# Kernel tuning notes

Measured on AMD Instinct MI355X. Metric: run time of the kernel, lower is better.

## Reference

```python
import jax, jax.numpy as jnp
import numpy as np
from jax.ops import segment_sum, segment_max

N_M = 100000   # muon nodes
N_J = 100000   # jet nodes
E   = 1600000  # edges per relation (~avg degree 16)
D   = 64       # input feature dim
H   = 64       # hidden_channels
C   = 2        # num_classes

def setup_inputs():
    key = jax.random.key(0)
    ks = jax.random.split(key, 16)
    g = lambda k, shape, fan: jax.random.normal(k, shape, jnp.float32) / np.sqrt(fan).astype(np.float32)
    return {
        "x_muons": jax.random.normal(ks[0], (N_M, D), jnp.float32),
        "x_jets":  jax.random.normal(ks[1], (N_J, D), jnp.float32),
        "ei_mm": jax.random.randint(ks[2], (2, E), 0, N_M, jnp.int32),
        "ei_mj": jnp.stack([jax.random.randint(ks[3], (E,), 0, N_M, jnp.int32),
                            jax.random.randint(ks[4], (E,), 0, N_J, jnp.int32)]),
        "ei_jj": jax.random.randint(ks[5], (2, E), 0, N_J, jnp.int32),
        "gat_w_src": g(ks[6], (D, H), D),
        "gat_w_dst": g(ks[7], (D, H), D),
        "gat_att_src": g(ks[8], (H,), H),
        "gat_att_dst": g(ks[9], (H,), H),
        "gat_bias": jnp.zeros((H,), jnp.float32),
        "sage_w_l": g(ks[10], (D, H), D),
        "sage_w_r": g(ks[11], (D, H), D),
        "sage_bias": jnp.zeros((H,), jnp.float32),
        "gcn_w": g(ks[12], (D, H), D),
        "gcn_bias": jnp.zeros((H,), jnp.float32),
        "lin_w": g(ks[13], (H, C), H),
        "lin_b": jnp.zeros((C,), jnp.float32),
    }

def _add_self_loops(ei, n):
    loop = jnp.arange(n, dtype=ei.dtype)
    return jnp.concatenate([ei[0], loop]), jnp.concatenate([ei[1], loop])

def _gat(x, ei, w_src, w_dst, att_src, att_dst, bias):
    # PyG GATConv, heads=1, add_self_loops=True, negative_slope=0.2
    n = x.shape[0]
    src, dst = _add_self_loops(ei, n)
    hs = x @ w_src                      # [n, H] source-side messages
    hd = x @ w_dst                      # dst-side (attention only)
    a = jax.nn.leaky_relu((hs @ att_src)[src] + (hd @ att_dst)[dst], 0.2)
    m = segment_max(a, dst, num_segments=n)      # per-dst softmax (stable)
    ea = jnp.exp(a - m[dst])
    z = segment_sum(ea, dst, num_segments=n)
    alpha = ea / z[dst]                 # self loop guarantees z > 0
    return segment_sum(alpha[:, None] * hs[src], dst, num_segments=n) + bias

def _sage(x_src, x_dst, ei, w_l, w_r, bias):
    # PyG SAGEConv: mean aggregation, root weight, no self loops
    n = x_dst.shape[0]
    src, dst = ei[0], ei[1]
    agg = segment_sum(x_src[src], dst, num_segments=n)
    cnt = segment_sum(jnp.ones_like(dst, jnp.float32), dst, num_segments=n)
    mean = agg / jnp.maximum(cnt, 1.0)[:, None]
    return mean @ w_l + x_dst @ w_r + bias

def _gcn(x, ei, w, bias):
    # PyG GCNConv: symmetric gcn_norm on A + I
    n = x.shape[0]
    src, dst = _add_self_loops(ei, n)
    xw = x @ w
    deg = segment_sum(jnp.ones_like(dst, jnp.float32), dst, num_segments=n)
    dis = deg ** -0.5                   # deg >= 1 due to self loops
    norm = dis[src] * dis[dst]
    return segment_sum(norm[:, None] * xw[src], dst, num_segments=n) + bias

def reference(x_muons, x_jets, ei_mm, ei_mj, ei_jj,
              gat_w_src, gat_w_dst, gat_att_src, gat_att_dst, gat_bias,
              sage_w_l, sage_w_r, sage_bias, gcn_w, gcn_bias, lin_w, lin_b):
    # Original forward returns inside the layer loop -> exactly one HeteroConv layer runs.
    muons = _gat(x_muons, ei_mm, gat_w_src, gat_w_dst, gat_att_src, gat_att_dst, gat_bias)
    jets = (_sage(x_muons, x_jets, ei_mj, sage_w_l, sage_w_r, sage_bias)
            + _gcn(x_jets, ei_jj, gcn_w, gcn_bias))   # HeteroConv aggr='sum' on dst type 'jets'
    muons = jax.nn.relu(muons)
    jets = jax.nn.relu(jets)
    out = jnp.concatenate([muons, jets], axis=0)       # [N_M + N_J, H]
    return jax.nn.sigmoid(out @ lin_w + lin_b)
```

## Files before the change

### kernel.cpp

```cpp
#include <hip/hip_runtime.h>
#include <math.h>

#define N_M 100000
#define N_J 100000
#define NE  1600000
#define NTOT (3*N_M)
#define ETOT (3*NE)
#define NB_SCAN 293
#define DD  64
#define HH  64

#define NBIN 586
#define BIN_SHIFT 9
#define G1 640
#define EPB ((ETOT + G1 - 1) / G1)

__device__ __forceinline__ float lrelu(float a){ return a > 0.f ? a : 0.2f*a; }
__device__ __forceinline__ float wmax(float v){
    #pragma unroll
    for (int o = 32; o; o >>= 1) v = fmaxf(v, __shfl_xor(v, o));
    return v;
}
__device__ __forceinline__ float wsum(float v){
    #pragma unroll
    for (int o = 32; o; o >>= 1) v += __shfl_xor(v, o);
    return v;
}
__device__ __forceinline__ float sigm(float x){ return 1.f/(1.f + expf(-x)); }


__global__ void k_vdst(const float* __restrict__ w_dst, const float* __restrict__ att_dst,
                       float* __restrict__ v_dst){
    int d = threadIdx.x;
    float s = 0.f;
    for (int h = 0; h < HH; ++h) s += w_dst[d*HH + h] * att_dst[h];
    v_dst[d] = s;
}

__global__ __launch_bounds__(256) void k_muon_prep(
    const float* __restrict__ x, const float* __restrict__ w_src,
    const float* __restrict__ att_src, const float* __restrict__ v_dst,
    float* __restrict__ hs, float* __restrict__ as_, float* __restrict__ ad_)
{
    __shared__ float lw[DD*HH];
    __shared__ float latt[HH];
    __shared__ float lvd[DD];
    int tid = threadIdx.x;
    for (int i = tid; i < DD*HH; i += 256) lw[i] = w_src[i];
    if (tid < HH) latt[tid] = att_src[tid];
    if (tid < DD) lvd[tid] = v_dst[tid];
    __syncthreads();
    int row = blockIdx.x*64 + (tid >> 2);
    int q = tid & 3;
    if (row >= N_M) return;
    const float4* x4 = (const float4*)(x + (size_t)row*DD);
    float acc[16];
    #pragma unroll
    for (int f = 0; f < 16; ++f) acc[f] = 0.f;
    float adp = 0.f;
    for (int kk = 0; kk < 16; ++kk){
        float4 xv = x4[kk];
        adp += xv.x*lvd[4*kk] + xv.y*lvd[4*kk+1] + xv.z*lvd[4*kk+2] + xv.w*lvd[4*kk+3];
        float xs[4] = {xv.x, xv.y, xv.z, xv.w};
        #pragma unroll
        for (int j = 0; j < 4; ++j){
            const float* wp = lw + (4*kk + j)*HH + (q << 4);
            float xk = xs[j];
            #pragma unroll
            for (int f = 0; f < 16; ++f) acc[f] = fmaf(xk, wp[f], acc[f]);
        }
    }
    float asp = 0.f;
    #pragma unroll
    for (int f = 0; f < 16; ++f) asp += acc[f] * latt[(q<<4) + f];
    asp += __shfl_xor(asp, 1);
    asp += __shfl_xor(asp, 2);
    float* hp = hs + (size_t)row*HH + (q << 4);
    #pragma unroll
    for (int j = 0; j < 4; ++j)
        ((float4*)hp)[j] = make_float4(acc[4*j], acc[4*j+1], acc[4*j+2], acc[4*j+3]);
    if (q == 0){ as_[row] = asp; ad_[row] = adp; }
}

__global__ __launch_bounds__(256) void k_gcn_xw(
    const float* __restrict__ x, const float* __restrict__ w, float* __restrict__ xw)
{
    __shared__ float lw[DD*HH];
    int tid = threadIdx.x;
    for (int i = tid; i < DD*HH; i += 256) lw[i] = w[i];
    __syncthreads();
    int row = blockIdx.x*64 + (tid >> 2);
    int q = tid & 3;
    if (row >= N_J) return;
    const float4* x4 = (const float4*)(x + (size_t)row*DD);
    float acc[16];
    #pragma unroll
    for (int f = 0; f < 16; ++f) acc[f] = 0.f;
    for (int kk = 0; kk < 16; ++kk){
        float4 xv = x4[kk];
        float xs[4] = {xv.x, xv.y, xv.z, xv.w};
        #pragma unroll
        for (int j = 0; j < 4; ++j){
            const float* wp = lw + (4*kk + j)*HH + (q << 4);
            float xk = xs[j];
            #pragma unroll
            for (int f = 0; f < 16; ++f) acc[f] = fmaf(xk, wp[f], acc[f]);
        }
    }
    float* hp = xw + (size_t)row*HH + (q << 4);
    #pragma unroll
    for (int j = 0; j < 4; ++j)
        ((float4*)hp)[j] = make_float4(acc[4*j], acc[4*j+1], acc[4*j+2], acc[4*j+3]);
}


__device__ __forceinline__ void edge_rd(int t, const int* ei_mm, const int* ei_mj,
                                        const int* ei_jj, const int** ei, int* r, int* e){
    if (t < NE){ *r = 0; *e = t; *ei = ei_mm; }
    else if (t < 2*NE){ *r = 1; *e = t - NE; *ei = ei_mj; }
    else { *r = 2; *e = t - 2*NE; *ei = ei_jj; }
}

__global__ __launch_bounds__(256) void k_bin0(
    const int* __restrict__ ei_mm, const int* __restrict__ ei_mj,
    const int* __restrict__ ei_jj, int* __restrict__ g_bincnt)
{
    __shared__ int bh[NBIN];
    int tid = threadIdx.x;
    for (int i = tid; i < NBIN; i += 256) bh[i] = 0;
    __syncthreads();
    int t0 = blockIdx.x * EPB;
    int t1 = min(t0 + EPB, ETOT);
    for (int t = t0 + tid; t < t1; t += 256){
        const int* ei; int r, e;
        edge_rd(t, ei_mm, ei_mj, ei_jj, &ei, &r, &e);
        int bucket = r*N_M + ei[NE + e];
        atomicAdd(&bh[bucket >> BIN_SHIFT], 1);
    }
    __syncthreads();
    for (int i = tid; i < NBIN; i += 256)
        if (bh[i]) atomicAdd(&g_bincnt[i], bh[i]);
}

__global__ void k_binscan(const int* __restrict__ g_bincnt, int* __restrict__ g_binoff,
                          int* __restrict__ g_bincur, int* __restrict__ offs)
{
    int l = threadIdx.x;
    int base = l * 10;
    int v[10]; int s = 0;
    #pragma unroll
    for (int k = 0; k < 10; ++k){
        int idx = base + k;
        v[k] = (idx < NBIN) ? g_bincnt[idx] : 0;
        s += v[k];
    }
    int inc = s;
    #pragma unroll
    for (int o = 1; o < 64; o <<= 1){
        int u = __shfl_up(inc, o);
        if (l >= o) inc += u;
    }
    int ex = inc - s;
    #pragma unroll
    for (int k = 0; k < 10; ++k){
        int idx = base + k;
        if (idx < NBIN){ g_binoff[idx] = ex; g_bincur[idx] = ex; ex += v[k]; }
    }
    if (l == 63) g_binoff[NBIN] = ex;
    if (l == 0)  offs[NTOT] = ETOT;
}

__global__ __launch_bounds__(256) void k_bin1(
    const int* __restrict__ ei_mm, const int* __restrict__ ei_mj,
    const int* __restrict__ ei_jj, int* __restrict__ g_bincur,
    unsigned* __restrict__ binned)
{
    __shared__ int bh[NBIN];
    __shared__ int cb[NBIN];
    int tid = threadIdx.x;
    for (int i = tid; i < NBIN; i += 256) bh[i] = 0;
    __syncthreads();
    int t0 = blockIdx.x * EPB;
    int t1 = min(t0 + EPB, ETOT);
    for (int t = t0 + tid; t < t1; t += 256){
        const int* ei; int r, e;
        edge_rd(t, ei_mm, ei_mj, ei_jj, &ei, &r, &e);
        int bucket = r*N_M + ei[NE + e];
        atomicAdd(&bh[bucket >> BIN_SHIFT], 1);
    }
    __syncthreads();
    for (int i = tid; i < NBIN; i += 256){
        int c = bh[i];
        cb[i] = c ? atomicAdd(&g_bincur[i], c) : 0;
        bh[i] = 0;
    }
    __syncthreads();
    for (int t = t0 + tid; t < t1; t += 256){
        const int* ei; int r, e;
        edge_rd(t, ei_mm, ei_mj, ei_jj, &ei, &r, &e);
        int s = ei[e];
        int bucket = r*N_M + ei[NE + e];
        int bin = bucket >> BIN_SHIFT;
        int lb  = bucket & 511;
        int pos = cb[bin] + atomicAdd(&bh[bin], 1);
        binned[pos] = ((unsigned)lb << 17) | (unsigned)s;
    }
}

__global__ __launch_bounds__(256) void k_build(
    const unsigned* __restrict__ binned, const int* __restrict__ g_binoff,
    int* __restrict__ offs, int* __restrict__ perm)
{
    __shared__ int lh[512];
    __shared__ int lcur[512];
    __shared__ int ls[256];
    int b = blockIdx.x, tid = threadIdx.x;
    int e0 = g_binoff[b], e1 = g_binoff[b+1];
    lh[tid] = 0; lh[tid + 256] = 0;
    __syncthreads();
    for (int e = e0 + tid; e < e1; e += 256)
        atomicAdd(&lh[binned[e] >> 17], 1);
    __syncthreads();
    int a0 = lh[2*tid], a1 = lh[2*tid + 1];
    int s = a0 + a1;
    ls[tid] = s; __syncthreads();
    for (int o = 1; o < 256; o <<= 1){
        int u = (tid >= o) ? ls[tid - o] : 0;
        __syncthreads();
        ls[tid] += u;
        __syncthreads();
    }
    int ex = ls[tid] - s;
    lcur[2*tid]     = ex;
    lcur[2*tid + 1] = ex + a0;
    int gb = b*512 + 2*tid;
    if (gb     < NTOT) offs[gb]     = e0 + ex;
    if (gb + 1 < NTOT) offs[gb + 1] = e0 + ex + a0;
    __syncthreads();
    for (int e = e0 + tid; e < e1; e += 256){
        unsigned p = binned[e];
        int pos = atomicAdd(&lcur[p >> 17], 1);
        perm[e0 + pos] = (int)(p & 0x1FFFFu);
    }
}


__global__ void k_hist(const int* __restrict__ ei_mm, const int* __restrict__ ei_mj,
                       const int* __restrict__ ei_jj, int* __restrict__ cnt){
    int t = blockIdx.x*256 + threadIdx.x;
    if (t >= ETOT) return;
    const int* ei; int r, e;
    edge_rd(t, ei_mm, ei_mj, ei_jj, &ei, &r, &e);
    atomicAdd(&cnt[r*N_M + ei[NE + e]], 1);
}

__global__ __launch_bounds__(256) void k_scan1(const int* __restrict__ cnt,
                                               int* __restrict__ offs, int* __restrict__ bsum){
    __shared__ int ls[256];
    int b = blockIdx.x, t = threadIdx.x;
    int base = b*1024 + t*4;
    int4 c = make_int4(0,0,0,0);
    if (base < NTOT) c = *(const int4*)(cnt + base);
    int s = c.x + c.y + c.z + c.w;
    ls[t] = s; __syncthreads();
    for (int o = 1; o < 256; o <<= 1){
        int a = (t >= o) ? ls[t - o] : 0;
        __syncthreads();
        ls[t] += a;
        __syncthreads();
    }
    int excl = ls[t] - s;
    if (t == 255) bsum[b] = ls[255];
    if (base < NTOT){
        offs[base]   = excl;
        offs[base+1] = excl + c.x;
        offs[base+2] = excl + c.x + c.y;
        offs[base+3] = excl + c.x + c.y + c.z;
    }
}

__global__ __launch_bounds__(512) void k_scan2(int* __restrict__ bsum){
    __shared__ int ls[512];
    int t = threadIdx.x;
    int v = (t < NB_SCAN) ? bsum[t] : 0;
    ls[t] = v; __syncthreads();
    for (int o = 1; o < 512; o <<= 1){
        int a = (t >= o) ? ls[t - o] : 0;
        __syncthreads();
        ls[t] += a;
        __syncthreads();
    }
    if (t < NB_SCAN) bsum[t] = ls[t] - v;
}

__global__ void k_scan3(int* __restrict__ offs, const int* __restrict__ bsum){
    int b = blockIdx.x, t = threadIdx.x;
    int base = b*1024 + t*4;
    if (base >= NTOT) return;
    int add = bsum[b];
    int4* p = (int4*)(offs + base);
    int4 v = *p;
    v.x += add; v.y += add; v.z += add; v.w += add;
    *p = v;
}

__global__ void k_fill(const int* __restrict__ ei_mm, const int* __restrict__ ei_mj,
                       const int* __restrict__ ei_jj, const int* __restrict__ offs,
                       int* __restrict__ cursor, int* __restrict__ perm){
    int t = blockIdx.x*256 + threadIdx.x;
    if (t >= ETOT) return;
    const int* ei; int r, e;
    edge_rd(t, ei_mm, ei_mj, ei_jj, &ei, &r, &e);
    int s = ei[e];
    int bkt = r*N_M + ei[NE + e];
    int pos = atomicAdd(&cursor[bkt], 1);
    perm[offs[bkt] + pos] = s;
}

__global__ void k_set_offs_top(int* __restrict__ offs){ offs[NTOT] = ETOT; }

__global__ void k_dis(const int* __restrict__ offs, float* __restrict__ dis){
    int j = blockIdx.x*256 + threadIdx.x;
    if (j >= N_J) return;
    int beg = offs[2*N_M + j];
    int end = (j == N_J-1) ? ETOT : offs[2*N_M + j + 1];
    dis[j] = rsqrtf((float)(end - beg + 1));
}


__global__ __launch_bounds__(256) void k_muon_gat_out(
    const int* __restrict__ offs, const int* __restrict__ perm,
    const float* __restrict__ as_, const float* __restrict__ ad_,
    const float* __restrict__ hs, const float* __restrict__ gat_bias,
    const float* __restrict__ lin_w, const float* __restrict__ lin_b,
    float* __restrict__ out)
{
    int wid = threadIdx.x >> 6;
    int l = threadIdx.x & 63;
    int d = blockIdx.x*4 + wid;
    if (d >= N_M) return;
    int beg = offs[d], end = offs[d+1];
    float ad_d = ad_[d];
    float a_self = lrelu(as_[d] + ad_d);
    float am = a_self;
    for (int base = beg; base < end; base += 64){
        int e = base + l;
        if (e < end) am = fmaxf(am, lrelu(as_[perm[e]] + ad_d));
    }
    float m = wmax(am);
    float eself = expf(a_self - m);
    float z = eself;
    float acc0 = eself * hs[(size_t)d*HH + l], acc1 = 0.f;
    for (int base = beg; base < end; base += 64){
        int e = base + l;
        int sB = 0; float eaB = 0.f;
        if (e < end){
            sB = perm[e];
            eaB = expf(lrelu(as_[sB] + ad_d) - m);
        }
        z += wsum(eaB);
        int cc = min(64, end - base);
        int k = 0;
        for (; k + 8 <= cc; k += 8){
            int s0=__shfl(sB,k+0), s1=__shfl(sB,k+1), s2=__shfl(sB,k+2), s3=__shfl(sB,k+3);
            int s4=__shfl(sB,k+4), s5=__shfl(sB,k+5), s6=__shfl(sB,k+6), s7=__shfl(sB,k+7);
            float e0=__shfl(eaB,k+0), e1=__shfl(eaB,k+1), e2=__shfl(eaB,k+2), e3=__shfl(eaB,k+3);
            float e4=__shfl(eaB,k+4), e5=__shfl(eaB,k+5), e6=__shfl(eaB,k+6), e7=__shfl(eaB,k+7);
            float v0=hs[(size_t)s0*HH+l], v1=hs[(size_t)s1*HH+l];
            float v2=hs[(size_t)s2*HH+l], v3=hs[(size_t)s3*HH+l];
            float v4=hs[(size_t)s4*HH+l], v5=hs[(size_t)s5*HH+l];
            float v6=hs[(size_t)s6*HH+l], v7=hs[(size_t)s7*HH+l];
            acc0 = fmaf(e0,v0,acc0); acc1 = fmaf(e1,v1,acc1);
            acc0 = fmaf(e2,v2,acc0); acc1 = fmaf(e3,v3,acc1);
            acc0 = fmaf(e4,v4,acc0); acc1 = fmaf(e5,v5,acc1);
            acc0 = fmaf(e6,v6,acc0); acc1 = fmaf(e7,v7,acc1);
        }
        for (; k < cc; ++k){
            int sk = __shfl(sB, k);
            float eak = __shfl(eaB, k);
            acc0 = fmaf(eak, hs[(size_t)sk*HH + l], acc0);
        }
    }
    float val = fmaxf((acc0 + acc1) / z + gat_bias[l], 0.f);
    float p0 = wsum(val * lin_w[l*2 + 0]);
    float p1 = wsum(val * lin_w[l*2 + 1]);
    if (l == 0){
        size_t o = (size_t)d*2;
        out[o]   = sigm(p0 + lin_b[0]);
        out[o+1] = sigm(p1 + lin_b[1]);
    }
}

__global__ __launch_bounds__(512) void k_jet_out(
    const float* __restrict__ x_jets, const float* __restrict__ x_muons,
    const float* __restrict__ xw, const float* __restrict__ dis,
    const int* __restrict__ offs, const int* __restrict__ perm,
    const float* __restrict__ w_l, const float* __restrict__ w_r,
    const float* __restrict__ sage_bias, const float* __restrict__ gcn_bias,
    const float* __restrict__ lin_w, const float* __restrict__ lin_b,
    float* __restrict__ out)
{
    __shared__ float lwl[DD*HH];
    __shared__ float lwr[DD*HH];
    int tid = threadIdx.x;
    for (int i = tid; i < DD*HH; i += 512){ lwl[i] = w_l[i]; lwr[i] = w_r[i]; }
    __syncthreads();
    int wid = tid >> 6;
    int l = tid & 63;
    int j = blockIdx.x*8 + wid;
    if (j >= N_J) return;
    int beg = offs[N_M + j], end = offs[N_M + j + 1];
    float sa0 = 0.f, sa1 = 0.f;
    for (int base = beg; base < end; base += 64){
        int e = base + l;
        int sB = (e < end) ? perm[e] : 0;
        int cc = min(64, end - base);
        int k = 0;
        for (; k + 8 <= cc; k += 8){
            int s0=__shfl(sB,k+0), s1=__shfl(sB,k+1), s2=__shfl(sB,k+2), s3=__shfl(sB,k+3);
            int s4=__shfl(sB,k+4), s5=__shfl(sB,k+5), s6=__shfl(sB,k+6), s7=__shfl(sB,k+7);
            float v0=x_muons[(size_t)s0*DD+l], v1=x_muons[(size_t)s1*DD+l];
            float v2=x_muons[(size_t)s2*DD+l], v3=x_muons[(size_t)s3*DD+l];
            float v4=x_muons[(size_t)s4*DD+l], v5=x_muons[(size_t)s5*DD+l];
            float v6=x_muons[(size_t)s6*DD+l], v7=x_muons[(size_t)s7*DD+l];
            sa0 += v0 + v2; sa1 += v1 + v3;
            sa0 += v4 + v6; sa1 += v5 + v7;
        }
        for (; k < cc; ++k){
            int sk = __shfl(sB, k);
            sa0 += x_muons[(size_t)sk*DD + l];
        }
    }
    float inv = (end > beg) ? 1.f/(float)(end - beg) : 1.f;
    float mean = (sa0 + sa1) * inv;
    int beg2 = offs[2*N_M + j];
    int end2 = (j == N_J-1) ? ETOT : offs[2*N_M + j + 1];
    float dj = dis[j];
    float g0 = dj*dj*xw[(size_t)j*HH + l], g1 = 0.f;
    for (int base = beg2; base < end2; base += 64){
        int e = base + l;
        int sB = 0; float nB = 0.f;
        if (e < end2){ sB = perm[e]; nB = dis[sB]*dj; }
        int cc = min(64, end2 - base);
        int k = 0;
        for (; k + 8 <= cc; k += 8){
            int s0=__shfl(sB,k+0), s1=__shfl(sB,k+1), s2=__shfl(sB,k+2), s3=__shfl(sB,k+3);
            int s4=__shfl(sB,k+4), s5=__shfl(sB,k+5), s6=__shfl(sB,k+6), s7=__shfl(sB,k+7);
            float n0=__shfl(nB,k+0), n1=__shfl(nB,k+1), n2=__shfl(nB,k+2), n3=__shfl(nB,k+3);
            float n4=__shfl(nB,k+4), n5=__shfl(nB,k+5), n6=__shfl(nB,k+6), n7=__shfl(nB,k+7);
            float v0=xw[(size_t)s0*HH+l], v1=xw[(size_t)s1*HH+l];
            float v2=xw[(size_t)s2*HH+l], v3=xw[(size_t)s3*HH+l];
            float v4=xw[(size_t)s4*HH+l], v5=xw[(size_t)s5*HH+l];
            float v6=xw[(size_t)s6*HH+l], v7=xw[(size_t)s7*HH+l];
            g0 = fmaf(n0,v0,g0); g1 = fmaf(n1,v1,g1);
            g0 = fmaf(n2,v2,g0); g1 = fmaf(n3,v3,g1);
            g0 = fmaf(n4,v4,g0); g1 = fmaf(n5,v5,g1);
            g0 = fmaf(n6,v6,g0); g1 = fmaf(n7,v7,g1);
        }
        for (; k < cc; ++k){
            int sk = __shfl(sB, k);
            float nk = __shfl(nB, k);
            g0 = fmaf(nk, xw[(size_t)sk*HH + l], g0);
        }
    }
    float xv = x_jets[(size_t)j*DD + l];
    float accf = g0 + g1 + gcn_bias[l] + sage_bias[l];
    for (int k = 0; k < 64; ++k){
        float mk = __shfl(mean, k);
        float xk = __shfl(xv, k);
        accf = fmaf(mk, lwl[k*64 + l], fmaf(xk, lwr[k*64 + l], accf));
    }
    float val = fmaxf(accf, 0.f);
    float p0 = wsum(val * lin_w[l*2 + 0]);
    float p1 = wsum(val * lin_w[l*2 + 1]);
    if (l == 0){
        size_t o = (size_t)(N_M + j)*2;
        out[o]   = sigm(p0 + lin_b[0]);
        out[o+1] = sigm(p1 + lin_b[1]);
    }
}

extern "C" void kernel_launch(void* const* d_in, const int* in_sizes, int n_in,
                              void* d_out, int out_size, void* d_ws, size_t ws_size,
                              hipStream_t stream) {
    const float* x_muons   = (const float*)d_in[0];
    const float* x_jets    = (const float*)d_in[1];
    const int*   ei_mm     = (const int*)d_in[2];
    const int*   ei_mj     = (const int*)d_in[3];
    const int*   ei_jj     = (const int*)d_in[4];
    const float* gat_w_src = (const float*)d_in[5];
    const float* gat_w_dst = (const float*)d_in[6];
    const float* gat_att_s = (const float*)d_in[7];
    const float* gat_att_d = (const float*)d_in[8];
    const float* gat_bias  = (const float*)d_in[9];
    const float* sage_w_l  = (const float*)d_in[10];
    const float* sage_w_r  = (const float*)d_in[11];
    const float* sage_bias = (const float*)d_in[12];
    const float* gcn_w     = (const float*)d_in[13];
    const float* gcn_bias  = (const float*)d_in[14];
    const float* lin_w     = (const float*)d_in[15];
    const float* lin_b     = (const float*)d_in[16];
    float* out = (float*)d_out;

    float* ws = (float*)d_ws;
    size_t o = 0;
    float* hs    = ws + o; o += (size_t)N_M*HH;
    float* as_   = ws + o; o += N_M;
    float* ad_   = ws + o; o += N_M;
    float* xw    = ws + o; o += (size_t)N_J*HH;
    float* dis   = ws + o; o += N_J;
    float* v_dst = ws + o; o += 64;
    int* offs   = (int*)(ws + o); o += NTOT + 4;
    int* perm   = (int*)(ws + o); o += ETOT;
    size_t o_common = o;

    int nb64_m = (N_M + 63) / 64;
    int nb64_j = (N_J + 63) / 64;

    k_vdst<<<1, 64, 0, stream>>>(gat_w_dst, gat_att_d, v_dst);
    k_muon_prep<<<nb64_m, 256, 0, stream>>>(x_muons, gat_w_src, gat_att_s, v_dst, hs, as_, ad_);
    k_gcn_xw<<<nb64_j, 256, 0, stream>>>(x_jets, gcn_w, xw);

    size_t need_fast = (o_common + ETOT + 3*NBIN + 16) * sizeof(float);
    if (ws_size >= need_fast){
        unsigned* binned = (unsigned*)(ws + o); o += ETOT;
        int* g_bincnt    = (int*)(ws + o); o += NBIN;
        int* g_binoff    = (int*)(ws + o); o += NBIN + 4;
        int* g_bincur    = (int*)(ws + o); o += NBIN;
        hipMemsetAsync(g_bincnt, 0, NBIN*sizeof(int), stream);
        k_bin0<<<G1, 256, 0, stream>>>(ei_mm, ei_mj, ei_jj, g_bincnt);
        k_binscan<<<1, 64, 0, stream>>>(g_bincnt, g_binoff, g_bincur, offs);
        k_bin1<<<G1, 256, 0, stream>>>(ei_mm, ei_mj, ei_jj, g_bincur, binned);
        k_build<<<NBIN, 256, 0, stream>>>(binned, g_binoff, offs, perm);
    } else {
        int* cnt    = (int*)(ws + o); o += NTOT;
        int* cursor = (int*)(ws + o); o += NTOT;
        int* bsum   = (int*)(ws + o); o += 512;
        hipMemsetAsync(cnt,    0, (size_t)NTOT*sizeof(int), stream);
        hipMemsetAsync(cursor, 0, (size_t)NTOT*sizeof(int), stream);
        int nbE3 = (ETOT + 255) / 256;
        k_hist<<<nbE3, 256, 0, stream>>>(ei_mm, ei_mj, ei_jj, cnt);
        k_scan1<<<NB_SCAN, 256, 0, stream>>>(cnt, offs, bsum);
        k_scan2<<<1, 512, 0, stream>>>(bsum);
        k_scan3<<<NB_SCAN, 256, 0, stream>>>(offs, bsum);
        k_fill<<<nbE3, 256, 0, stream>>>(ei_mm, ei_mj, ei_jj, offs, cursor, perm);
        k_set_offs_top<<<1, 1, 0, stream>>>(offs);
    }

    k_dis<<<(N_J + 255)/256, 256, 0, stream>>>(offs, dis);

    k_muon_gat_out<<<N_M/4, 256, 0, stream>>>(offs, perm, as_, ad_, hs,
                                              gat_bias, lin_w, lin_b, out);
    k_jet_out<<<(N_J + 7)/8, 512, 0, stream>>>(x_jets, x_muons, xw, dis, offs, perm,
                                               sage_w_l, sage_w_r, sage_bias, gcn_bias,
                                               lin_w, lin_b, out);
}
```

Baseline: 509.6 us.

## Store gathered node features in bf16 and merge muon/jet output kernels

The projected muon features, GCN projected jet features, and raw muon features used by SAGE are now stored as bf16, which halves the bytes per random gather in the edge aggregation loops. A new conversion kernel produces the bf16 copy of x_muons. The separate muon GAT and jet output kernels are merged into one launch with interleaved block roles, so both halves can overlap on the GPU. Precision drops to bf16 for the gathered values, which adds rounding error.

```diff
diff --git a/kernel.cpp b/kernel.cpp
--- a/kernel.cpp
+++ b/kernel.cpp
@@ -28,6 +28,15 @@
 }
 __device__ __forceinline__ float sigm(float x){ return 1.f/(1.f + expf(-x)); }
 
+__device__ __forceinline__ unsigned short f2bf(float f){
+    unsigned u = __float_as_uint(f);
+    u += 0x7FFFu + ((u >> 16) & 1u);
+    return (unsigned short)(u >> 16);
+}
+__device__ __forceinline__ float bf2f(unsigned short h){
+    return __uint_as_float((unsigned)h << 16);
+}
+
 
 __global__ void k_vdst(const float* __restrict__ w_dst, const float* __restrict__ att_dst,
                        float* __restrict__ v_dst){
@@ -40,7 +49,7 @@
 __global__ __launch_bounds__(256) void k_muon_prep(
     const float* __restrict__ x, const float* __restrict__ w_src,
     const float* __restrict__ att_src, const float* __restrict__ v_dst,
-    float* __restrict__ hs, float* __restrict__ as_, float* __restrict__ ad_)
+    unsigned short* __restrict__ hs_b, float* __restrict__ as_, float* __restrict__ ad_)
 {
     __shared__ float lw[DD*HH];
     __shared__ float latt[HH];
@@ -75,15 +84,16 @@
     for (int f = 0; f < 16; ++f) asp += acc[f] * latt[(q<<4) + f];
     asp += __shfl_xor(asp, 1);
     asp += __shfl_xor(asp, 2);
-    float* hp = hs + (size_t)row*HH + (q << 4);
+    unsigned short* hp = hs_b + (size_t)row*HH + (q << 4);
     #pragma unroll
     for (int j = 0; j < 4; ++j)
-        ((float4*)hp)[j] = make_float4(acc[4*j], acc[4*j+1], acc[4*j+2], acc[4*j+3]);
+        ((ushort4*)hp)[j] = make_ushort4(f2bf(acc[4*j]), f2bf(acc[4*j+1]),
+                                         f2bf(acc[4*j+2]), f2bf(acc[4*j+3]));
     if (q == 0){ as_[row] = asp; ad_[row] = adp; }
 }
 
 __global__ __launch_bounds__(256) void k_gcn_xw(
-    const float* __restrict__ x, const float* __restrict__ w, float* __restrict__ xw)
+    const float* __restrict__ x, const float* __restrict__ w, unsigned short* __restrict__ xw_b)
 {
     __shared__ float lw[DD*HH];
     int tid = threadIdx.x;
@@ -107,10 +117,18 @@
             for (int f = 0; f < 16; ++f) acc[f] = fmaf(xk, wp[f], acc[f]);
         }
     }
-    float* hp = xw + (size_t)row*HH + (q << 4);
+    unsigned short* hp = xw_b + (size_t)row*HH + (q << 4);
     #pragma unroll
     for (int j = 0; j < 4; ++j)
-        ((float4*)hp)[j] = make_float4(acc[4*j], acc[4*j+1], acc[4*j+2], acc[4*j+3]);
+        ((ushort4*)hp)[j] = make_ushort4(f2bf(acc[4*j]), f2bf(acc[4*j+1]),
+                                         f2bf(acc[4*j+2]), f2bf(acc[4*j+3]));
+}
+
+__global__ void k_xm(const float* __restrict__ x, unsigned short* __restrict__ xb){
+    int i = blockIdx.x*256 + threadIdx.x;
+    if (i >= N_M*DD/4) return;
+    float4 v = ((const float4*)x)[i];
+    ((ushort4*)xb)[i] = make_ushort4(f2bf(v.x), f2bf(v.y), f2bf(v.z), f2bf(v.w));
 }
 
 
@@ -328,73 +346,12 @@
 }
 
 
-__global__ __launch_bounds__(256) void k_muon_gat_out(
+__global__ __launch_bounds__(512) void k_out(
+    const float* __restrict__ x_jets, const unsigned short* __restrict__ xm_b,
+    const unsigned short* __restrict__ xw_b, const float* __restrict__ dis,
     const int* __restrict__ offs, const int* __restrict__ perm,
     const float* __restrict__ as_, const float* __restrict__ ad_,
-    const float* __restrict__ hs, const float* __restrict__ gat_bias,
-    const float* __restrict__ lin_w, const float* __restrict__ lin_b,
-    float* __restrict__ out)
-{
-    int wid = threadIdx.x >> 6;
-    int l = threadIdx.x & 63;
-    int d = blockIdx.x*4 + wid;
-    if (d >= N_M) return;
-    int beg = offs[d], end = offs[d+1];
-    float ad_d = ad_[d];
-    float a_self = lrelu(as_[d] + ad_d);
-    float am = a_self;
-    for (int base = beg; base < end; base += 64){
-        int e = base + l;
-        if (e < end) am = fmaxf(am, lrelu(as_[perm[e]] + ad_d));
-    }
-    float m = wmax(am);
-    float eself = expf(a_self - m);
-    float z = eself;
-    float acc0 = eself * hs[(size_t)d*HH + l], acc1 = 0.f;
-    for (int base = beg; base < end; base += 64){
-        int e = base + l;
-        int sB = 0; float eaB = 0.f;
-        if (e < end){
-            sB = perm[e];
-            eaB = expf(lrelu(as_[sB] + ad_d) - m);
-        }
-        z += wsum(eaB);
-        int cc = min(64, end - base);
-        int k = 0;
-        for (; k + 8 <= cc; k += 8){
-            int s0=__shfl(sB,k+0), s1=__shfl(sB,k+1), s2=__shfl(sB,k+2), s3=__shfl(sB,k+3);
-            int s4=__shfl(sB,k+4), s5=__shfl(sB,k+5), s6=__shfl(sB,k+6), s7=__shfl(sB,k+7);
-            float e0=__shfl(eaB,k+0), e1=__shfl(eaB,k+1), e2=__shfl(eaB,k+2), e3=__shfl(eaB,k+3);
-            float e4=__shfl(eaB,k+4), e5=__shfl(eaB,k+5), e6=__shfl(eaB,k+6), e7=__shfl(eaB,k+7);
-            float v0=hs[(size_t)s0*HH+l], v1=hs[(size_t)s1*HH+l];
-            float v2=hs[(size_t)s2*HH+l], v3=hs[(size_t)s3*HH+l];
-            float v4=hs[(size_t)s4*HH+l], v5=hs[(size_t)s5*HH+l];
-            float v6=hs[(size_t)s6*HH+l], v7=hs[(size_t)s7*HH+l];
-            acc0 = fmaf(e0,v0,acc0); acc1 = fmaf(e1,v1,acc1);
-            acc0 = fmaf(e2,v2,acc0); acc1 = fmaf(e3,v3,acc1);
-            acc0 = fmaf(e4,v4,acc0); acc1 = fmaf(e5,v5,acc1);
-            acc0 = fmaf(e6,v6,acc0); acc1 = fmaf(e7,v7,acc1);
-        }
-        for (; k < cc; ++k){
-            int sk = __shfl(sB, k);
-            float eak = __shfl(eaB, k);
-            acc0 = fmaf(eak, hs[(size_t)sk*HH + l], acc0);
-        }
-    }
-    float val = fmaxf((acc0 + acc1) / z + gat_bias[l], 0.f);
-    float p0 = wsum(val * lin_w[l*2 + 0]);
-    float p1 = wsum(val * lin_w[l*2 + 1]);
-    if (l == 0){
-        size_t o = (size_t)d*2;
-        out[o]   = sigm(p0 + lin_b[0]);
-        out[o+1] = sigm(p1 + lin_b[1]);
-    }
-}
-
-__global__ __launch_bounds__(512) void k_jet_out(
-    const float* __restrict__ x_jets, const float* __restrict__ x_muons,
-    const float* __restrict__ xw, const float* __restrict__ dis,
-    const int* __restrict__ offs, const int* __restrict__ perm,
+    const unsigned short* __restrict__ hs_b, const float* __restrict__ gat_bias,
     const float* __restrict__ w_l, const float* __restrict__ w_r,
     const float* __restrict__ sage_bias, const float* __restrict__ gcn_bias,
     const float* __restrict__ lin_w, const float* __restrict__ lin_b,
@@ -403,80 +360,136 @@
     __shared__ float lwl[DD*HH];
     __shared__ float lwr[DD*HH];
     int tid = threadIdx.x;
-    for (int i = tid; i < DD*HH; i += 512){ lwl[i] = w_l[i]; lwr[i] = w_r[i]; }
-    __syncthreads();
     int wid = tid >> 6;
     int l = tid & 63;
-    int j = blockIdx.x*8 + wid;
-    if (j >= N_J) return;
-    int beg = offs[N_M + j], end = offs[N_M + j + 1];
-    float sa0 = 0.f, sa1 = 0.f;
-    for (int base = beg; base < end; base += 64){
-        int e = base + l;
-        int sB = (e < end) ? perm[e] : 0;
-        int cc = min(64, end - base);
-        int k = 0;
-        for (; k + 8 <= cc; k += 8){
-            int s0=__shfl(sB,k+0), s1=__shfl(sB,k+1), s2=__shfl(sB,k+2), s3=__shfl(sB,k+3);
-            int s4=__shfl(sB,k+4), s5=__shfl(sB,k+5), s6=__shfl(sB,k+6), s7=__shfl(sB,k+7);
-            float v0=x_muons[(size_t)s0*DD+l], v1=x_muons[(size_t)s1*DD+l];
-            float v2=x_muons[(size_t)s2*DD+l], v3=x_muons[(size_t)s3*DD+l];
-            float v4=x_muons[(size_t)s4*DD+l], v5=x_muons[(size_t)s5*DD+l];
-            float v6=x_muons[(size_t)s6*DD+l], v7=x_muons[(size_t)s7*DD+l];
-            sa0 += v0 + v2; sa1 += v1 + v3;
-            sa0 += v4 + v6; sa1 += v5 + v7;
-        }
-        for (; k < cc; ++k){
-            int sk = __shfl(sB, k);
-            sa0 += x_muons[(size_t)sk*DD + l];
-        }
-    }
-    float inv = (end > beg) ? 1.f/(float)(end - beg) : 1.f;
-    float mean = (sa0 + sa1) * inv;
-    int beg2 = offs[2*N_M + j];
-    int end2 = (j == N_J-1) ? ETOT : offs[2*N_M + j + 1];
-    float dj = dis[j];
-    float g0 = dj*dj*xw[(size_t)j*HH + l], g1 = 0.f;
-    for (int base = beg2; base < end2; base += 64){
-        int e = base + l;
-        int sB = 0; float nB = 0.f;
-        if (e < end2){ sB = perm[e]; nB = dis[sB]*dj; }
-        int cc = min(64, end2 - base);
-        int k = 0;
-        for (; k + 8 <= cc; k += 8){
-            int s0=__shfl(sB,k+0), s1=__shfl(sB,k+1), s2=__shfl(sB,k+2), s3=__shfl(sB,k+3);
-            int s4=__shfl(sB,k+4), s5=__shfl(sB,k+5), s6=__shfl(sB,k+6), s7=__shfl(sB,k+7);
-            float n0=__shfl(nB,k+0), n1=__shfl(nB,k+1), n2=__shfl(nB,k+2), n3=__shfl(nB,k+3);
-            float n4=__shfl(nB,k+4), n5=__shfl(nB,k+5), n6=__shfl(nB,k+6), n7=__shfl(nB,k+7);
-            float v0=xw[(size_t)s0*HH+l], v1=xw[(size_t)s1*HH+l];
-            float v2=xw[(size_t)s2*HH+l], v3=xw[(size_t)s3*HH+l];
-            float v4=xw[(size_t)s4*HH+l], v5=xw[(size_t)s5*HH+l];
-            float v6=xw[(size_t)s6*HH+l], v7=xw[(size_t)s7*HH+l];
-            g0 = fmaf(n0,v0,g0); g1 = fmaf(n1,v1,g1);
-            g0 = fmaf(n2,v2,g0); g1 = fmaf(n3,v3,g1);
-            g0 = fmaf(n4,v4,g0); g1 = fmaf(n5,v5,g1);
-            g0 = fmaf(n6,v6,g0); g1 = fmaf(n7,v7,g1);
-        }
-        for (; k < cc; ++k){
-            int sk = __shfl(sB, k);
-            float nk = __shfl(nB, k);
-            g0 = fmaf(nk, xw[(size_t)sk*HH + l], g0);
-        }
-    }
-    float xv = x_jets[(size_t)j*DD + l];
-    float accf = g0 + g1 + gcn_bias[l] + sage_bias[l];
-    for (int k = 0; k < 64; ++k){
-        float mk = __shfl(mean, k);
-        float xk = __shfl(xv, k);
-        accf = fmaf(mk, lwl[k*64 + l], fmaf(xk, lwr[k*64 + l], accf));
-    }
-    float val = fmaxf(accf, 0.f);
-    float p0 = wsum(val * lin_w[l*2 + 0]);
-    float p1 = wsum(val * lin_w[l*2 + 1]);
-    if (l == 0){
-        size_t o = (size_t)(N_M + j)*2;
-        out[o]   = sigm(p0 + lin_b[0]);
-        out[o+1] = sigm(p1 + lin_b[1]);
+    int b = blockIdx.x;
+    if ((b & 1) == 0){
+        for (int i = tid; i < DD*HH; i += 512){ lwl[i] = w_l[i]; lwr[i] = w_r[i]; }
+        __syncthreads();
+        int j = (b >> 1)*8 + wid;
+        if (j >= N_J) return;
+        int beg = offs[N_M + j], end = offs[N_M + j + 1];
+        float sa0 = 0.f, sa1 = 0.f;
+        for (int base = beg; base < end; base += 64){
+            int e = base + l;
+            int sB = (e < end) ? perm[e] : 0;
+            int cc = min(64, end - base);
+            int k = 0;
+            for (; k + 8 <= cc; k += 8){
+                int s0=__shfl(sB,k+0), s1=__shfl(sB,k+1), s2=__shfl(sB,k+2), s3=__shfl(sB,k+3);
+                int s4=__shfl(sB,k+4), s5=__shfl(sB,k+5), s6=__shfl(sB,k+6), s7=__shfl(sB,k+7);
+                float v0=bf2f(xm_b[(size_t)s0*DD+l]), v1=bf2f(xm_b[(size_t)s1*DD+l]);
+                float v2=bf2f(xm_b[(size_t)s2*DD+l]), v3=bf2f(xm_b[(size_t)s3*DD+l]);
+                float v4=bf2f(xm_b[(size_t)s4*DD+l]), v5=bf2f(xm_b[(size_t)s5*DD+l]);
+                float v6=bf2f(xm_b[(size_t)s6*DD+l]), v7=bf2f(xm_b[(size_t)s7*DD+l]);
+                sa0 += v0 + v2; sa1 += v1 + v3;
+                sa0 += v4 + v6; sa1 += v5 + v7;
+            }
+            for (; k < cc; ++k){
+                int sk = __shfl(sB, k);
+                sa0 += bf2f(xm_b[(size_t)sk*DD + l]);
+            }
+        }
+        float inv = (end > beg) ? 1.f/(float)(end - beg) : 1.f;
+        float mean = (sa0 + sa1) * inv;
+        int beg2 = offs[2*N_M + j];
+        int end2 = (j == N_J-1) ? ETOT : offs[2*N_M + j + 1];
+        float dj = dis[j];
+        float g0 = dj*dj*bf2f(xw_b[(size_t)j*HH + l]), g1 = 0.f;
+        for (int base = beg2; base < end2; base += 64){
+            int e = base + l;
+            int sB = 0; float nB = 0.f;
+            if (e < end2){ sB = perm[e]; nB = dis[sB]*dj; }
+            int cc = min(64, end2 - base);
+            int k = 0;
+            for (; k + 8 <= cc; k += 8){
+                int s0=__shfl(sB,k+0), s1=__shfl(sB,k+1), s2=__shfl(sB,k+2), s3=__shfl(sB,k+3);
+                int s4=__shfl(sB,k+4), s5=__shfl(sB,k+5), s6=__shfl(sB,k+6), s7=__shfl(sB,k+7);
+                float n0=__shfl(nB,k+0), n1=__shfl(nB,k+1), n2=__shfl(nB,k+2), n3=__shfl(nB,k+3);
+                float n4=__shfl(nB,k+4), n5=__shfl(nB,k+5), n6=__shfl(nB,k+6), n7=__shfl(nB,k+7);
+                float v0=bf2f(xw_b[(size_t)s0*HH+l]), v1=bf2f(xw_b[(size_t)s1*HH+l]);
+                float v2=bf2f(xw_b[(size_t)s2*HH+l]), v3=bf2f(xw_b[(size_t)s3*HH+l]);
+                float v4=bf2f(xw_b[(size_t)s4*HH+l]), v5=bf2f(xw_b[(size_t)s5*HH+l]);
+                float v6=bf2f(xw_b[(size_t)s6*HH+l]), v7=bf2f(xw_b[(size_t)s7*HH+l]);
+                g0 = fmaf(n0,v0,g0); g1 = fmaf(n1,v1,g1);
+                g0 = fmaf(n2,v2,g0); g1 = fmaf(n3,v3,g1);
+                g0 = fmaf(n4,v4,g0); g1 = fmaf(n5,v5,g1);
+                g0 = fmaf(n6,v6,g0); g1 = fmaf(n7,v7,g1);
+            }
+            for (; k < cc; ++k){
+                int sk = __shfl(sB, k);
+                float nk = __shfl(nB, k);
+                g0 = fmaf(nk, bf2f(xw_b[(size_t)sk*HH + l]), g0);
+            }
+        }
+        float xv = x_jets[(size_t)j*DD + l];
+        float accf = g0 + g1 + gcn_bias[l] + sage_bias[l];
+        for (int k = 0; k < 64; ++k){
+            float mk = __shfl(mean, k);
+            float xk = __shfl(xv, k);
+            accf = fmaf(mk, lwl[k*64 + l], fmaf(xk, lwr[k*64 + l], accf));
+        }
+        float val = fmaxf(accf, 0.f);
+        float p0 = wsum(val * lin_w[l*2 + 0]);
+        float p1 = wsum(val * lin_w[l*2 + 1]);
+        if (l == 0){
+            size_t o = (size_t)(N_M + j)*2;
+            out[o]   = sigm(p0 + lin_b[0]);
+            out[o+1] = sigm(p1 + lin_b[1]);
+        }
+    } else {
+        int d = (b >> 1)*8 + wid;
+        if (d >= N_M) return;
+        int beg = offs[d], end = offs[d+1];
+        float ad_d = ad_[d];
+        float a_self = lrelu(as_[d] + ad_d);
+        float am = a_self;
+        for (int base = beg; base < end; base += 64){
+            int e = base + l;
+            if (e < end) am = fmaxf(am, lrelu(as_[perm[e]] + ad_d));
+        }
+        float m = wmax(am);
+        float eself = expf(a_self - m);
+        float z = eself;
+        float acc0 = eself * bf2f(hs_b[(size_t)d*HH + l]), acc1 = 0.f;
+        for (int base = beg; base < end; base += 64){
+            int e = base + l;
+            int sB = 0; float eaB = 0.f;
+            if (e < end){
+                sB = perm[e];
+                eaB = expf(lrelu(as_[sB] + ad_d) - m);
+            }
+            z += wsum(eaB);
+            int cc = min(64, end - base);
+            int k = 0;
+            for (; k + 8 <= cc; k += 8){
+                int s0=__shfl(sB,k+0), s1=__shfl(sB,k+1), s2=__shfl(sB,k+2), s3=__shfl(sB,k+3);
+                int s4=__shfl(sB,k+4), s5=__shfl(sB,k+5), s6=__shfl(sB,k+6), s7=__shfl(sB,k+7);
+                float e0=__shfl(eaB,k+0), e1=__shfl(eaB,k+1), e2=__shfl(eaB,k+2), e3=__shfl(eaB,k+3);
+                float e4=__shfl(eaB,k+4), e5=__shfl(eaB,k+5), e6=__shfl(eaB,k+6), e7=__shfl(eaB,k+7);
+                float v0=bf2f(hs_b[(size_t)s0*HH+l]), v1=bf2f(hs_b[(size_t)s1*HH+l]);
+                float v2=bf2f(hs_b[(size_t)s2*HH+l]), v3=bf2f(hs_b[(size_t)s3*HH+l]);
+                float v4=bf2f(hs_b[(size_t)s4*HH+l]), v5=bf2f(hs_b[(size_t)s5*HH+l]);
+                float v6=bf2f(hs_b[(size_t)s6*HH+l]), v7=bf2f(hs_b[(size_t)s7*HH+l]);
+                acc0 = fmaf(e0,v0,acc0); acc1 = fmaf(e1,v1,acc1);
+                acc0 = fmaf(e2,v2,acc0); acc1 = fmaf(e3,v3,acc1);
+                acc0 = fmaf(e4,v4,acc0); acc1 = fmaf(e5,v5,acc1);
+                acc0 = fmaf(e6,v6,acc0); acc1 = fmaf(e7,v7,acc1);
+            }
+            for (; k < cc; ++k){
+                int sk = __shfl(sB, k);
+                float eak = __shfl(eaB, k);
+                acc0 = fmaf(eak, bf2f(hs_b[(size_t)sk*HH + l]), acc0);
+            }
+        }
+        float val = fmaxf((acc0 + acc1) / z + gat_bias[l], 0.f);
+        float p0 = wsum(val * lin_w[l*2 + 0]);
+        float p1 = wsum(val * lin_w[l*2 + 1]);
+        if (l == 0){
+            size_t o = (size_t)d*2;
+            out[o]   = sigm(p0 + lin_b[0]);
+            out[o+1] = sigm(p1 + lin_b[1]);
+        }
     }
 }
 
@@ -504,10 +517,11 @@
 
     float* ws = (float*)d_ws;
     size_t o = 0;
-    float* hs    = ws + o; o += (size_t)N_M*HH;
+    unsigned short* hs_b = (unsigned short*)(ws + o); o += (size_t)N_M*HH/2;
+    unsigned short* xw_b = (unsigned short*)(ws + o); o += (size_t)N_J*HH/2;
+    unsigned short* xm_b = (unsigned short*)(ws + o); o += (size_t)N_M*DD/2;
     float* as_   = ws + o; o += N_M;
     float* ad_   = ws + o; o += N_M;
-    float* xw    = ws + o; o += (size_t)N_J*HH;
     float* dis   = ws + o; o += N_J;
     float* v_dst = ws + o; o += 64;
     int* offs   = (int*)(ws + o); o += NTOT + 4;
@@ -518,8 +532,9 @@
     int nb64_j = (N_J + 63) / 64;
 
     k_vdst<<<1, 64, 0, stream>>>(gat_w_dst, gat_att_d, v_dst);
-    k_muon_prep<<<nb64_m, 256, 0, stream>>>(x_muons, gat_w_src, gat_att_s, v_dst, hs, as_, ad_);
-    k_gcn_xw<<<nb64_j, 256, 0, stream>>>(x_jets, gcn_w, xw);
+    k_muon_prep<<<nb64_m, 256, 0, stream>>>(x_muons, gat_w_src, gat_att_s, v_dst, hs_b, as_, ad_);
+    k_gcn_xw<<<nb64_j, 256, 0, stream>>>(x_jets, gcn_w, xw_b);
+    k_xm<<<(N_M*DD/4 + 255)/256, 256, 0, stream>>>(x_muons, xm_b);
 
     size_t need_fast = (o_common + ETOT + 3*NBIN + 16) * sizeof(float);
     if (ws_size >= need_fast){
@@ -549,9 +564,9 @@
 
     k_dis<<<(N_J + 255)/256, 256, 0, stream>>>(offs, dis);
 
-    k_muon_gat_out<<<N_M/4, 256, 0, stream>>>(offs, perm, as_, ad_, hs,
-                                              gat_bias, lin_w, lin_b, out);
-    k_jet_out<<<(N_J + 7)/8, 512, 0, stream>>>(x_jets, x_muons, xw, dis, offs, perm,
-                                               sage_w_l, sage_w_r, sage_bias, gcn_bias,
-                                               lin_w, lin_b, out);
-}
+    int nb_out = 2 * ((N_M + 7)/8);
+    k_out<<<nb_out, 512, 0, stream>>>(x_jets, xm_b, xw_b, dis, offs, perm,
+                                      as_, ad_, hs_b, gat_bias,
+                                      sage_w_l, sage_w_r, sage_bias, gcn_bias,
+                                      lin_w, lin_b, out);
+}
```

Result: slower. 675.6 us (+32.6%).
